# Performance work log

Hardware: AMD Instinct MI355X
Metric: run time of the kernel (lower is better)

The kernel has to match this reference:

```python
import jax, jax.numpy as jnp
import numpy as np

N, E = 10000, 100000   # nodes, edges
C = 64                 # sphere_channels
L2 = 9                 # (lmax+1)^2 with lmax=2
H, DH, DV = 8, 16, 16  # heads, alpha channels/head, value channels/head
EC = 64                # edge scalar channels
NRBF = 128             # radial basis size
ZMAX = 90              # max_num_elements


def setup_inputs() -> dict:
    key = jax.random.key(0)
    ks = jax.random.split(key, 12)
    inp = {}
    inp["node_embedding"] = jax.random.normal(ks[0], (N, L2, C), jnp.float32)
    inp["atomic_numbers"] = jax.random.randint(ks[1], (N,), 0, ZMAX)
    inp["edge_distance"] = jax.random.uniform(ks[2], (E,), jnp.float32)
    inp["edge_index"] = jax.random.randint(ks[3], (2, E), 0, N)
    # per-edge Wigner rotation into the edge-aligned SO(2) frame
    inp["wigner"] = jax.random.normal(ks[4], (E, L2, L2), jnp.float32) / np.sqrt(L2)
    # learned parameters
    inp["atom_emb"] = jax.random.normal(ks[5], (ZMAX, EC), jnp.float32) * 0.1
    inp["W_rbf"] = jax.random.normal(ks[6], (NRBF, EC), jnp.float32) / np.sqrt(NRBF)
    inp["W_gate"] = jax.random.normal(ks[7], (EC, H * DH), jnp.float32) / np.sqrt(EC)
    inp["W_msg"] = jax.random.normal(ks[8], (2 * C, H * DH), jnp.float32) / np.sqrt(2 * C)
    inp["alpha_vec"] = jax.random.normal(ks[9], (H, DH), jnp.float32) / np.sqrt(DH)
    inp["W_val"] = jax.random.normal(ks[10], (H * DH, H * DV), jnp.float32) / np.sqrt(H * DH)
    inp["W_out"] = jax.random.normal(ks[11], (H * DV, 1), jnp.float32) / np.sqrt(H * DV)
    return inp


def reference(node_embedding, atomic_numbers, edge_distance, edge_index, wigner,
              atom_emb, W_rbf, W_gate, W_msg, alpha_vec, W_val, W_out):
    src, dst = edge_index[0], edge_index[1]
    # --- edge scalar embedding: gaussian RBF of distance + endpoint atom embeddings ---
    centers = jnp.linspace(0.0, 1.0, NRBF, dtype=node_embedding.dtype)
    width = 1.0 / NRBF
    rbf = jnp.exp(-((edge_distance[:, None] - centers) ** 2) / (2.0 * width * width))  # [E, NRBF]
    edge_scalar = jax.nn.silu(rbf @ W_rbf + atom_emb[atomic_numbers[src]] + atom_emb[atomic_numbers[dst]])  # [E, EC]
    gate = jax.nn.silu(edge_scalar @ W_gate)  # [E, H*DH]
    # --- gather endpoint embeddings and rotate into edge frame (SO3 rotation) ---
    x_s = jnp.einsum('eij,ejc->eic', wigner, node_embedding[src])  # [E, L2, C]
    x_t = jnp.einsum('eij,ejc->eic', wigner, node_embedding[dst])  # [E, L2, C]
    msg = jnp.concatenate([x_s, x_t], axis=-1) @ W_msg            # [E, L2, H*DH]
    msg = msg * gate[:, None, :]
    # --- attention logits from the invariant (l=0) component ---
    a = msg[:, 0, :].reshape(E, H, DH)
    logits = jnp.einsum('ehd,hd->eh', jax.nn.leaky_relu(a, 0.2), alpha_vec)  # [E, H]
    # --- softmax over incoming edges of each destination node ---
    m = jax.ops.segment_max(logits, dst, num_segments=N)  # [N, H]
    ex = jnp.exp(logits - m[dst])
    den = jax.ops.segment_sum(ex, dst, num_segments=N)
    attn = ex / (den[dst] + 1e-9)  # [E, H]
    # --- attention-weighted values, rotate back, scatter-sum to nodes ---
    v = (msg @ W_val).reshape(E, L2, H, DV)
    v = v * attn[:, None, :, None]
    v = jnp.einsum('eji,ejhv->eihv', wigner, v).reshape(E, L2, H * DV)  # rotate back (R^T)
    node_out = jax.ops.segment_sum(v, dst, num_segments=N)  # [N, L2, H*DV]
    out = node_out @ W_out                                   # [N, L2, 1]
    forces = out[:, 1:4, 0]                                  # narrow(1,1,3).view(-1,3)
    return forces
```

## Files before the change

kernel.cpp:

```cpp
#include <hip/hip_runtime.h>
#include <hip/hip_bf16.h>

#define NN 10000
#define NE 100000

typedef __attribute__((ext_vector_type(8))) short short8v;
typedef __attribute__((ext_vector_type(4))) float float4v;

__device__ __forceinline__ unsigned int enc_f(float f) {
  unsigned int u = __float_as_uint(f);
  return (u & 0x80000000u) ? ~u : (u | 0x80000000u);
}
__device__ __forceinline__ float dec_f(unsigned int u) {
  return __uint_as_float((u & 0x80000000u) ? (u & 0x7fffffffu) : ~u);
}
__device__ __forceinline__ float silu_f(float x) {
  return x / (1.0f + __expf(-x));
}
__device__ __forceinline__ void f32_hilo(float x, short& h, short& l) {
  __hip_bfloat16 bh = __float2bfloat16(x);
  float r = x - __bfloat162float(bh);
  __hip_bfloat16 bl = __float2bfloat16(r);
  h = __builtin_bit_cast(short, bh);
  l = __builtin_bit_cast(short, bl);
}
#define MFMA16(a, b, c) __builtin_amdgcn_mfma_f32_16x16x32_bf16(a, b, c, 0, 0, 0)

__global__ void prep_kernel(const float* __restrict__ W_msg, const float* __restrict__ W_val,
                            const float* __restrict__ W_out, const float* __restrict__ W_rbf,
                            const float* __restrict__ W_gate,
                            float* __restrict__ Q,
                            short* __restrict__ Wp1h, short* __restrict__ Wp1l,
                            short* __restrict__ Wp2h, short* __restrict__ Wp2l,
                            short* __restrict__ Wp3h, short* __restrict__ Wp3l,
                            short* __restrict__ Wp4h, short* __restrict__ Wp4l) {
  int i = blockIdx.x * blockDim.x + threadIdx.x;
  if (i < 1024) {
    int c = i >> 3, h = i & 7;
    float s = 0.0f;
#pragma unroll
    for (int dv = 0; dv < 16; ++dv)
      s += W_val[c * 128 + h * 16 + dv] * W_out[h * 16 + dv];
    Q[c * 8 + h] = s;
  }
  const float* W; short* ph; short* pl; int KF, Nw, local; bool tr = false;
  if (i < 8192)       { W = W_rbf;  ph = Wp1h; pl = Wp1l; KF = 4; Nw = 64;  local = i; }
  else if (i < 16384) { W = W_gate; ph = Wp2h; pl = Wp2l; KF = 2; Nw = 128; local = i - 8192; }
  else if (i < 32768) { W = W_msg;  ph = Wp3h; pl = Wp3l; KF = 4; Nw = 128; local = i - 16384; }
  else                { W = W_msg;  ph = Wp4h; pl = Wp4l; KF = 4; Nw = 128; local = i - 32768; tr = true; }
  int tile = local >> 9;
  int ln = (local >> 3) & 63;
  int j = local & 7;
  int nt = tile / KF, kf = tile % KF;
  int k = kf * 32 + 8 * (ln >> 4) + j;
  int n = nt * 16 + (ln & 15);
  float w = tr ? W[n * 128 + k] : W[k * Nw + n];
  short h, lo;
  f32_hilo(w, h, lo);
  ph[local] = h;
  pl[local] = lo;
}

__global__ __launch_bounds__(256) void gather1_kernel(
    const float* __restrict__ nb, const int* __restrict__ ei,
    const float* __restrict__ wig, float* __restrict__ xc) {
  const int lane = threadIdx.x & 63;
  const int e = blockIdx.x * 4 + (threadIdx.x >> 6);
  int se = ei[e], de = ei[NE + e];
  const float* __restrict__ pw = wig + (size_t)e * 81;
  const float* __restrict__ ps = nb + (size_t)se * 576 + lane;
  const float* __restrict__ pt = nb + (size_t)de * 576 + lane;
  float vs[9], vt[9], wj[9];
#pragma unroll
  for (int j = 0; j < 9; ++j) {
    vs[j] = ps[j * 64];
    vt[j] = pt[j * 64];
    wj[j] = pw[j];
  }
  float xs = 0.0f, xt = 0.0f;
#pragma unroll
  for (int j = 0; j < 9; ++j) { xs += wj[j] * vs[j]; xt += wj[j] * vt[j]; }
  xc[(size_t)e * 128 + lane] = xs;
  xc[(size_t)e * 128 + 64 + lane] = xt;
}

__global__ __launch_bounds__(256, 3) void pass1_kernel(
    const int* __restrict__ zn, const float* __restrict__ dist,
    const int* __restrict__ ei, const float* __restrict__ aemb,
    const float* __restrict__ alpha, const float* __restrict__ xc,
    const short* __restrict__ Wp1h, const short* __restrict__ Wp1l,
    const short* __restrict__ Wp2h, const short* __restrict__ Wp2l,
    const short* __restrict__ Wp3h, const short* __restrict__ Wp3l,
    float* __restrict__ logits, unsigned int* __restrict__ m_enc,
    __hip_bfloat16* __restrict__ gate_ws) {
  __shared__ __attribute__((aligned(16))) float es_s[4][16][68];
  const int tid = threadIdx.x;
  const int lane = tid & 63;
  const int wid = tid >> 6;
  const int g = lane >> 4;
  const int col = lane & 15;
  const int e0 = (blockIdx.x * 4 + wid) * 16;

  int l16 = lane & 15;
  int ecl16 = (e0 + l16 < NE) ? e0 + l16 : NE - 1;
  int idx_v = 0;
  if (lane < 32) idx_v = ei[(lane < 16 ? 0 : NE) + ecl16];

  int ecol = e0 + col; if (ecol >= NE) ecol = NE - 1;
  const float d = dist[ecol];

  const float* __restrict__ xr = xc + (size_t)ecol * 128;
  float4v xv[4][2];
#pragma unroll
  for (int kf = 0; kf < 4; ++kf) {
    xv[kf][0] = *(const float4v*)(xr + kf * 32 + 8 * g);
    xv[kf][1] = *(const float4v*)(xr + kf * 32 + 8 * g + 4);
  }

  short8v a1h[4], a1l[4];
#pragma unroll
  for (int kf = 0; kf < 4; ++kf) {
#pragma unroll
    for (int j = 0; j < 8; ++j) {
      int k = kf * 32 + 8 * g + j;
      float t = d - (float)k * (1.0f / 127.0f);
      float v = __expf(-8192.0f * t * t);
      short h, lo; f32_hilo(v, h, lo);
      a1h[kf][j] = h; a1l[kf][j] = lo;
    }
  }

  const float4v z4 = {0.0f, 0.0f, 0.0f, 0.0f};

  float4v acc1[4];
#pragma unroll
  for (int nt = 0; nt < 4; ++nt) {
    float4v a = z4;
#pragma unroll
    for (int kf = 0; kf < 4; ++kf) {
      short8v bh = *(const short8v*)(Wp1h + ((nt * 4 + kf) * 64 + lane) * 8);
      short8v bl = *(const short8v*)(Wp1l + ((nt * 4 + kf) * 64 + lane) * 8);
      a = MFMA16(a1h[kf], bh, a);
      a = MFMA16(a1h[kf], bl, a);
      a = MFMA16(a1l[kf], bh, a);
    }
    acc1[nt] = a;
  }

  int dn_r[4];
#pragma unroll
  for (int r = 0; r < 4; ++r) {
    int sn = __shfl(idx_v, 4 * g + r);
    dn_r[r] = __shfl(idx_v, 16 + 4 * g + r);
    int zs = zn[sn], zd = zn[dn_r[r]];
#pragma unroll
    for (int nt = 0; nt < 4; ++nt) {
      float b = aemb[zs * 64 + nt * 16 + col] + aemb[zd * 64 + nt * 16 + col];
      es_s[wid][4 * g + r][nt * 16 + col] = silu_f(acc1[nt][r] + b);
    }
  }

  short8v a2h[2], a2l[2];
#pragma unroll
  for (int kf = 0; kf < 2; ++kf) {
    const float* p = &es_s[wid][col][kf * 32 + 8 * g];
    float4v v0 = *(const float4v*)p;
    float4v v1 = *(const float4v*)(p + 4);
#pragma unroll
    for (int j = 0; j < 4; ++j) {
      short h, lo;
      f32_hilo(v0[j], h, lo); a2h[kf][j] = h;     a2l[kf][j] = lo;
      f32_hilo(v1[j], h, lo); a2h[kf][4 + j] = h; a2l[kf][4 + j] = lo;
    }
  }

  float gate_r[8][4];
#pragma unroll
  for (int nt = 0; nt < 8; ++nt) {
    float4v a = z4;
#pragma unroll
    for (int kf = 0; kf < 2; ++kf) {
      short8v bh = *(const short8v*)(Wp2h + ((nt * 2 + kf) * 64 + lane) * 8);
      short8v bl = *(const short8v*)(Wp2l + ((nt * 2 + kf) * 64 + lane) * 8);
      a = MFMA16(a2h[kf], bh, a);
      a = MFMA16(a2h[kf], bl, a);
      a = MFMA16(a2l[kf], bh, a);
    }
#pragma unroll
    for (int r = 0; r < 4; ++r) {
      float gv = silu_f(a[r]);
      gate_r[nt][r] = gv;
      int er = e0 + 4 * g + r;
      if (er < NE)
        gate_ws[(size_t)er * 128 + nt * 16 + col] = __float2bfloat16(gv);
    }
  }

  short8v a3h[4], a3l[4];
#pragma unroll
  for (int kf = 0; kf < 4; ++kf) {
#pragma unroll
    for (int j = 0; j < 4; ++j) {
      short h, lo;
      f32_hilo(xv[kf][0][j], h, lo); a3h[kf][j] = h;     a3l[kf][j] = lo;
      f32_hilo(xv[kf][1][j], h, lo); a3h[kf][4 + j] = h; a3l[kf][4 + j] = lo;
    }
  }

#pragma unroll
  for (int nt = 0; nt < 8; ++nt) {
    float4v a = z4;
#pragma unroll
    for (int kf = 0; kf < 4; ++kf) {
      short8v bh = *(const short8v*)(Wp3h + ((nt * 4 + kf) * 64 + lane) * 8);
      short8v bl = *(const short8v*)(Wp3l + ((nt * 4 + kf) * 64 + lane) * 8);
      a = MFMA16(a3h[kf], bh, a);
      a = MFMA16(a3h[kf], bl, a);
      a = MFMA16(a3l[kf], bh, a);
    }
    float al = alpha[nt * 16 + col];
#pragma unroll
    for (int r = 0; r < 4; ++r) {
      float v = a[r] * gate_r[nt][r];
      v = v > 0.0f ? v : 0.2f * v;
      v *= al;
#pragma unroll
      for (int off = 1; off < 16; off <<= 1) v += __shfl_xor(v, off);
      int er = e0 + 4 * g + r;
      if (col == 0 && er < NE) {
        logits[(size_t)er * 8 + nt] = v;
        atomicMax(&m_enc[dn_r[r] * 8 + nt], enc_f(v));
      }
    }
  }
}

__global__ void pass2_kernel(const float* __restrict__ logits,
                             const int* __restrict__ ei,
                             const unsigned int* __restrict__ m_enc,
                             float* __restrict__ den) {
  int i = blockIdx.x * blockDim.x + threadIdx.x;
  if (i >= NE * 8) return;
  int e = i >> 3, h = i & 7;
  int dn = ei[NE + e];
  float mm = dec_f(m_enc[dn * 8 + h]);
  atomicAdd(&den[dn * 8 + h], __expf(logits[i] - mm));
}

__global__ __launch_bounds__(256, 3) void pass3a_kernel(
    const int* __restrict__ ei, const float* __restrict__ logits,
    const unsigned int* __restrict__ m_enc, const float* __restrict__ den,
    const __hip_bfloat16* __restrict__ gate_ws, const float* __restrict__ Q,
    const short* __restrict__ Wp4h, const short* __restrict__ Wp4l,
    float* __restrict__ t_ws) {
  __shared__ __attribute__((aligned(16))) float attn_s[4][16][8];
  __shared__ __attribute__((aligned(16))) float x_s[4][16][132];
  const int tid = threadIdx.x;
  const int lane = tid & 63;
  const int wid = tid >> 6;
  const int g = lane >> 4;
  const int col = lane & 15;
  const int e0 = (blockIdx.x * 4 + wid) * 16;

#pragma unroll
  for (int half = 0; half < 2; ++half) {
    int i = half * 64 + lane;
    int e = i >> 3, h = i & 7;
    int ec = e0 + e; if (ec >= NE) ec = NE - 1;
    int dn = ei[NE + ec];
    float l = logits[(size_t)ec * 8 + h];
    float mm = dec_f(m_enc[dn * 8 + h]);
    float dv = den[dn * 8 + h];
    attn_s[wid][e][h] = __expf(l - mm) / (dv + 1e-9f);
  }

  float q0[8], q1[8];
#pragma unroll
  for (int h = 0; h < 8; ++h) {
    q0[h] = Q[(2 * lane) * 8 + h];
    q1[h] = Q[(2 * lane + 1) * 8 + h];
  }
#pragma unroll 4
  for (int e = 0; e < 16; ++e) {
    int ec = e0 + e; if (ec >= NE) ec = NE - 1;
    float4v a0 = *(const float4v*)&attn_s[wid][e][0];
    float4v a1 = *(const float4v*)&attn_s[wid][e][4];
    float wv0 = 0.0f, wv1 = 0.0f;
#pragma unroll
    for (int h = 0; h < 4; ++h) {
      wv0 += q0[h] * a0[h] + q0[4 + h] * a1[h];
      wv1 += q1[h] * a0[h] + q1[4 + h] * a1[h];
    }
    unsigned int gp = *(const unsigned int*)(gate_ws + (size_t)ec * 128 + 2 * lane);
    float gg0 = __uint_as_float((gp & 0xffffu) << 16);
    float gg1 = __uint_as_float((gp & 0xffff0000u));
    float2 uu; uu.x = gg0 * wv0; uu.y = gg1 * wv1;
    *(float2*)&x_s[wid][e][2 * lane] = uu;
  }

  short8v ah[4], al[4];
#pragma unroll
  for (int kf = 0; kf < 4; ++kf) {
    const float* p = &x_s[wid][col][kf * 32 + 8 * g];
    float4v v0 = *(const float4v*)p;
    float4v v1 = *(const float4v*)(p + 4);
#pragma unroll
    for (int j = 0; j < 4; ++j) {
      short h, lo;
      f32_hilo(v0[j], h, lo); ah[kf][j] = h;     al[kf][j] = lo;
      f32_hilo(v1[j], h, lo); ah[kf][4 + j] = h; al[kf][4 + j] = lo;
    }
  }
  const float4v z4 = {0.0f, 0.0f, 0.0f, 0.0f};
#pragma unroll
  for (int nt = 0; nt < 8; ++nt) {
    float4v a = z4;
#pragma unroll
    for (int kf = 0; kf < 4; ++kf) {
      short8v bh = *(const short8v*)(Wp4h + ((nt * 4 + kf) * 64 + lane) * 8);
      short8v bl = *(const short8v*)(Wp4l + ((nt * 4 + kf) * 64 + lane) * 8);
      a = MFMA16(ah[kf], bh, a);
      a = MFMA16(ah[kf], bl, a);
      a = MFMA16(al[kf], bh, a);
    }
#pragma unroll
    for (int r = 0; r < 4; ++r) {
      int er = e0 + 4 * g + r;
      if (er < NE)
        t_ws[(size_t)er * 128 + nt * 16 + col] = a[r];
    }
  }
}

__global__ __launch_bounds__(256) void pass3b_kernel(
    const float* __restrict__ nb, const int* __restrict__ ei,
    const float* __restrict__ wig, const float* __restrict__ t_ws,
    float* __restrict__ out) {
  const int lane = threadIdx.x & 63;
  const int e = blockIdx.x * 4 + (threadIdx.x >> 6);
  int se = ei[e], de = ei[NE + e];
  float t0 = t_ws[(size_t)e * 128 + lane];
  float t1 = t_ws[(size_t)e * 128 + 64 + lane];
  const float* __restrict__ ps = nb + (size_t)se * 576 + lane;
  const float* __restrict__ pt = nb + (size_t)de * 576 + lane;
  float p[9];
#pragma unroll
  for (int j = 0; j < 9; ++j)
    p[j] = ps[j * 64] * t0 + pt[j * 64] * t1;
#pragma unroll
  for (int off = 1; off < 64; off <<= 1)
#pragma unroll
    for (int j = 0; j < 9; ++j) p[j] += __shfl_xor(p[j], off);

  const float* __restrict__ we = wig + (size_t)e * 81;
  int ls = lane < 9 ? lane : 8;
  float s_l = 0.0f;
#pragma unroll
  for (int jp = 0; jp < 9; ++jp) s_l += we[ls * 9 + jp] * p[jp];
  int lc = (lane >= 1 && lane <= 3) ? lane : 1;
  float f = 0.0f;
#pragma unroll
  for (int j = 0; j < 9; ++j)
    f += __shfl(s_l, j) * we[j * 9 + lc];
  if (lane >= 1 && lane <= 3)
    atomicAdd(&out[de * 3 + (lane - 1)], f);
}

extern "C" void kernel_launch(void* const* d_in, const int* in_sizes, int n_in,
                              void* d_out, int out_size, void* d_ws, size_t ws_size,
                              hipStream_t stream) {
  const float* nb = (const float*)d_in[0];
  const int* zn = (const int*)d_in[1];
  const float* dist = (const float*)d_in[2];
  const int* ei = (const int*)d_in[3];
  const float* wig = (const float*)d_in[4];
  const float* aemb = (const float*)d_in[5];
  const float* W_rbf = (const float*)d_in[6];
  const float* W_gate = (const float*)d_in[7];
  const float* W_msg = (const float*)d_in[8];
  const float* alpha = (const float*)d_in[9];
  const float* W_val = (const float*)d_in[10];
  const float* W_out = (const float*)d_in[11];
  float* out = (float*)d_out;

  char* p = (char*)d_ws;
  float* Q = (float*)p;                   p += 1024 * 4;
  unsigned int* m_enc = (unsigned int*)p; p += (size_t)NN * 8 * 4;
  float* den = (float*)p;                 p += (size_t)NN * 8 * 4;
  float* logits = (float*)p;              p += (size_t)NE * 8 * 4;
  __hip_bfloat16* gate_ws = (__hip_bfloat16*)p; p += (size_t)NE * 128 * 2;
  short* Wp1h = (short*)p; p += 8192 * 2;
  short* Wp1l = (short*)p; p += 8192 * 2;
  short* Wp2h = (short*)p; p += 8192 * 2;
  short* Wp2l = (short*)p; p += 8192 * 2;
  short* Wp3h = (short*)p; p += 16384 * 2;
  short* Wp3l = (short*)p; p += 16384 * 2;
  short* Wp4h = (short*)p; p += 16384 * 2;
  short* Wp4l = (short*)p; p += 16384 * 2;
  float* xc_ws = (float*)p;               p += (size_t)NE * 128 * 4;
  float* t_ws = xc_ws;

  hipMemsetAsync(d_out, 0, (size_t)NN * 3 * 4, stream);
  hipMemsetAsync(m_enc, 0, (size_t)NN * 8 * 4, stream);
  hipMemsetAsync(den, 0, (size_t)NN * 8 * 4, stream);

  prep_kernel<<<192, 256, 0, stream>>>(W_msg, W_val, W_out, W_rbf, W_gate, Q,
                                       Wp1h, Wp1l, Wp2h, Wp2l, Wp3h, Wp3l, Wp4h, Wp4l);
  gather1_kernel<<<NE / 4, 256, 0, stream>>>(nb, ei, wig, xc_ws);
  pass1_kernel<<<(NE + 63) / 64, 256, 0, stream>>>(zn, dist, ei, aemb, alpha, xc_ws,
                                                   Wp1h, Wp1l, Wp2h, Wp2l, Wp3h, Wp3l,
                                                   logits, m_enc, gate_ws);
  pass2_kernel<<<(NE * 8 + 255) / 256, 256, 0, stream>>>(logits, ei, m_enc, den);
  pass3a_kernel<<<(NE + 63) / 64, 256, 0, stream>>>(ei, logits, m_enc, den,
                                                    gate_ws, Q, Wp4h, Wp4l, t_ws);
  pass3b_kernel<<<NE / 4, 256, 0, stream>>>(nb, ei, wig, t_ws, out);
}
```

Before: 344.6 us.

## Precompute rotated Gram terms in gather and fuse pass3b into pass3

The gather kernel now computes the full rotated embedding for each edge. It writes the l=0 row as pre-split bf16 hi/lo pairs, and it writes the contraction of the rotated rows with Wigner columns 1..3 as a bf16 G tensor. This lets the final pass compute forces from G and the t-vector held in shared memory. The separate pass3b kernel, which re-gathered node embeddings and Wigner rows, is removed along with the t_ws round trip. This trades more FLOPs and an extra 768 B/edge of G writes in gather for removing a full endpoint re-gather, and it adds bf16 rounding on G.

```diff
diff --git a/kernel.cpp b/kernel.cpp
--- a/kernel.cpp
+++ b/kernel.cpp
@@ -5,6 +5,7 @@
 #define NE 100000
 
 typedef __attribute__((ext_vector_type(8))) short short8v;
+typedef __attribute__((ext_vector_type(4))) short short4v;
 typedef __attribute__((ext_vector_type(4))) float float4v;
 
 __device__ __forceinline__ unsigned int enc_f(float f) {
@@ -16,6 +17,9 @@
 }
 __device__ __forceinline__ float silu_f(float x) {
   return x / (1.0f + __expf(-x));
+}
+__device__ __forceinline__ float b2f(short s) {
+  return __uint_as_float(((unsigned int)(unsigned short)s) << 16);
 }
 __device__ __forceinline__ void f32_hilo(float x, short& h, short& l) {
   __hip_bfloat16 bh = __float2bfloat16(x);
@@ -23,6 +27,9 @@
   __hip_bfloat16 bl = __float2bfloat16(r);
   h = __builtin_bit_cast(short, bh);
   l = __builtin_bit_cast(short, bl);
+}
+__device__ __forceinline__ short f2bf(float x) {
+  return __builtin_bit_cast(short, __float2bfloat16(x));
 }
 #define MFMA16(a, b, c) __builtin_amdgcn_mfma_f32_16x16x32_bf16(a, b, c, 0, 0, 0)
 
@@ -63,31 +70,55 @@
 
 __global__ __launch_bounds__(256) void gather1_kernel(
     const float* __restrict__ nb, const int* __restrict__ ei,
-    const float* __restrict__ wig, float* __restrict__ xc) {
+    const float* __restrict__ wig, short* __restrict__ xch,
+    short* __restrict__ xcl, short* __restrict__ Gb) {
   const int lane = threadIdx.x & 63;
   const int e = blockIdx.x * 4 + (threadIdx.x >> 6);
   int se = ei[e], de = ei[NE + e];
   const float* __restrict__ pw = wig + (size_t)e * 81;
   const float* __restrict__ ps = nb + (size_t)se * 576 + lane;
   const float* __restrict__ pt = nb + (size_t)de * 576 + lane;
-  float vs[9], vt[9], wj[9];
+  float vs[9], vt[9];
 #pragma unroll
   for (int j = 0; j < 9; ++j) {
     vs[j] = ps[j * 64];
     vt[j] = pt[j * 64];
-    wj[j] = pw[j];
-  }
-  float xs = 0.0f, xt = 0.0f;
-#pragma unroll
-  for (int j = 0; j < 9; ++j) { xs += wj[j] * vs[j]; xt += wj[j] * vt[j]; }
-  xc[(size_t)e * 128 + lane] = xs;
-  xc[(size_t)e * 128 + 64 + lane] = xt;
+  }
+  float Gs0 = 0, Gs1 = 0, Gs2 = 0, Gt0 = 0, Gt1 = 0, Gt2 = 0;
+#pragma unroll
+  for (int j = 0; j < 9; ++j) {
+    float row[9];
+#pragma unroll
+    for (int jp = 0; jp < 9; ++jp) row[jp] = pw[j * 9 + jp];
+    float xs = 0.0f, xt = 0.0f;
+#pragma unroll
+    for (int jp = 0; jp < 9; ++jp) { xs += row[jp] * vs[jp]; xt += row[jp] * vt[jp]; }
+    if (j == 0) {
+      short h, l;
+      f32_hilo(xs, h, l);
+      xch[(size_t)e * 128 + lane] = h;
+      xcl[(size_t)e * 128 + lane] = l;
+      f32_hilo(xt, h, l);
+      xch[(size_t)e * 128 + 64 + lane] = h;
+      xcl[(size_t)e * 128 + 64 + lane] = l;
+    }
+    Gs0 += row[1] * xs; Gs1 += row[2] * xs; Gs2 += row[3] * xs;
+    Gt0 += row[1] * xt; Gt1 += row[2] * xt; Gt2 += row[3] * xt;
+  }
+  short* gp = Gb + (size_t)e * 384 + lane;
+  gp[0]       = f2bf(Gs0);
+  gp[64]      = f2bf(Gs1);
+  gp[128]     = f2bf(Gs2);
+  gp[192]     = f2bf(Gt0);
+  gp[256]     = f2bf(Gt1);
+  gp[320]     = f2bf(Gt2);
 }
 
 __global__ __launch_bounds__(256, 3) void pass1_kernel(
     const int* __restrict__ zn, const float* __restrict__ dist,
     const int* __restrict__ ei, const float* __restrict__ aemb,
-    const float* __restrict__ alpha, const float* __restrict__ xc,
+    const float* __restrict__ alpha,
+    const short* __restrict__ xch, const short* __restrict__ xcl,
     const short* __restrict__ Wp1h, const short* __restrict__ Wp1l,
     const short* __restrict__ Wp2h, const short* __restrict__ Wp2l,
     const short* __restrict__ Wp3h, const short* __restrict__ Wp3l,
@@ -109,12 +140,13 @@
   int ecol = e0 + col; if (ecol >= NE) ecol = NE - 1;
   const float d = dist[ecol];
 
-  const float* __restrict__ xr = xc + (size_t)ecol * 128;
-  float4v xv[4][2];
+  const short* ph = xch + (size_t)ecol * 128 + 8 * g;
+  const short* pl = xcl + (size_t)ecol * 128 + 8 * g;
+  short8v a3h[4], a3l[4];
 #pragma unroll
   for (int kf = 0; kf < 4; ++kf) {
-    xv[kf][0] = *(const float4v*)(xr + kf * 32 + 8 * g);
-    xv[kf][1] = *(const float4v*)(xr + kf * 32 + 8 * g + 4);
+    a3h[kf] = *(const short8v*)(ph + kf * 32);
+    a3l[kf] = *(const short8v*)(pl + kf * 32);
   }
 
   short8v a1h[4], a1l[4];
@@ -193,17 +225,6 @@
       int er = e0 + 4 * g + r;
       if (er < NE)
         gate_ws[(size_t)er * 128 + nt * 16 + col] = __float2bfloat16(gv);
-    }
-  }
-
-  short8v a3h[4], a3l[4];
-#pragma unroll
-  for (int kf = 0; kf < 4; ++kf) {
-#pragma unroll
-    for (int j = 0; j < 4; ++j) {
-      short h, lo;
-      f32_hilo(xv[kf][0][j], h, lo); a3h[kf][j] = h;     a3l[kf][j] = lo;
-      f32_hilo(xv[kf][1][j], h, lo); a3h[kf][4 + j] = h; a3l[kf][4 + j] = lo;
     }
   }
 
@@ -247,12 +268,12 @@
   atomicAdd(&den[dn * 8 + h], __expf(logits[i] - mm));
 }
 
-__global__ __launch_bounds__(256, 3) void pass3a_kernel(
+__global__ __launch_bounds__(256, 3) void pass3_kernel(
     const int* __restrict__ ei, const float* __restrict__ logits,
     const unsigned int* __restrict__ m_enc, const float* __restrict__ den,
     const __hip_bfloat16* __restrict__ gate_ws, const float* __restrict__ Q,
     const short* __restrict__ Wp4h, const short* __restrict__ Wp4l,
-    float* __restrict__ t_ws) {
+    const short* __restrict__ Gb, float* __restrict__ out) {
   __shared__ __attribute__((aligned(16))) float attn_s[4][16][8];
   __shared__ __attribute__((aligned(16))) float x_s[4][16][132];
   const int tid = threadIdx.x;
@@ -324,46 +345,37 @@
       a = MFMA16(al[kf], bh, a);
     }
 #pragma unroll
-    for (int r = 0; r < 4; ++r) {
-      int er = e0 + 4 * g + r;
-      if (er < NE)
-        t_ws[(size_t)er * 128 + nt * 16 + col] = a[r];
-    }
-  }
-}
-
-__global__ __launch_bounds__(256) void pass3b_kernel(
-    const float* __restrict__ nb, const int* __restrict__ ei,
-    const float* __restrict__ wig, const float* __restrict__ t_ws,
-    float* __restrict__ out) {
-  const int lane = threadIdx.x & 63;
-  const int e = blockIdx.x * 4 + (threadIdx.x >> 6);
-  int se = ei[e], de = ei[NE + e];
-  float t0 = t_ws[(size_t)e * 128 + lane];
-  float t1 = t_ws[(size_t)e * 128 + 64 + lane];
-  const float* __restrict__ ps = nb + (size_t)se * 576 + lane;
-  const float* __restrict__ pt = nb + (size_t)de * 576 + lane;
-  float p[9];
-#pragma unroll
-  for (int j = 0; j < 9; ++j)
-    p[j] = ps[j * 64] * t0 + pt[j * 64] * t1;
-#pragma unroll
-  for (int off = 1; off < 64; off <<= 1)
-#pragma unroll
-    for (int j = 0; j < 9; ++j) p[j] += __shfl_xor(p[j], off);
-
-  const float* __restrict__ we = wig + (size_t)e * 81;
-  int ls = lane < 9 ? lane : 8;
-  float s_l = 0.0f;
-#pragma unroll
-  for (int jp = 0; jp < 9; ++jp) s_l += we[ls * 9 + jp] * p[jp];
-  int lc = (lane >= 1 && lane <= 3) ? lane : 1;
-  float f = 0.0f;
-#pragma unroll
-  for (int j = 0; j < 9; ++j)
-    f += __shfl(s_l, j) * we[j * 9 + lc];
-  if (lane >= 1 && lane <= 3)
-    atomicAdd(&out[de * 3 + (lane - 1)], f);
+    for (int r = 0; r < 4; ++r)
+      x_s[wid][4 * g + r][nt * 16 + col] = a[r];
+  }
+
+  const int cg = col * 4;
+#pragma unroll
+  for (int it = 0; it < 4; ++it) {
+    int e = it * 4 + g;
+    int eu = e0 + e;
+    bool valid = eu < NE;
+    int ec = valid ? eu : NE - 1;
+    int de = ei[NE + ec];
+    float4v t0 = *(const float4v*)&x_s[wid][e][cg];
+    float4v t1 = *(const float4v*)&x_s[wid][e][64 + cg];
+    const short* gp = Gb + (size_t)ec * 384 + cg;
+    float p[3];
+#pragma unroll
+    for (int i = 0; i < 3; ++i) {
+      short4v gs = *(const short4v*)(gp + i * 64);
+      short4v gt = *(const short4v*)(gp + (3 + i) * 64);
+      p[i] = b2f(gs[0]) * t0[0] + b2f(gs[1]) * t0[1] + b2f(gs[2]) * t0[2] + b2f(gs[3]) * t0[3] +
+             b2f(gt[0]) * t1[0] + b2f(gt[1]) * t1[1] + b2f(gt[2]) * t1[2] + b2f(gt[3]) * t1[3];
+    }
+#pragma unroll
+    for (int i = 0; i < 3; ++i)
+#pragma unroll
+      for (int off = 1; off < 16; off <<= 1) p[i] += __shfl_xor(p[i], off);
+    float pv = (col == 1) ? p[0] : ((col == 2) ? p[1] : p[2]);
+    if (valid && col >= 1 && col <= 3)
+      atomicAdd(&out[de * 3 + (col - 1)], pv);
+  }
 }
 
 extern "C" void kernel_launch(void* const* d_in, const int* in_sizes, int n_in,
@@ -397,8 +409,9 @@
   short* Wp3l = (short*)p; p += 16384 * 2;
   short* Wp4h = (short*)p; p += 16384 * 2;
   short* Wp4l = (short*)p; p += 16384 * 2;
-  float* xc_ws = (float*)p;               p += (size_t)NE * 128 * 4;
-  float* t_ws = xc_ws;
+  short* xch = (short*)p;                 p += (size_t)NE * 128 * 2;
+  short* xcl = (short*)p;                 p += (size_t)NE * 128 * 2;
+  short* Gb = (short*)p;                  p += (size_t)NE * 384 * 2;
 
   hipMemsetAsync(d_out, 0, (size_t)NN * 3 * 4, stream);
   hipMemsetAsync(m_enc, 0, (size_t)NN * 8 * 4, stream);
@@ -406,12 +419,12 @@
 
   prep_kernel<<<192, 256, 0, stream>>>(W_msg, W_val, W_out, W_rbf, W_gate, Q,
                                        Wp1h, Wp1l, Wp2h, Wp2l, Wp3h, Wp3l, Wp4h, Wp4l);
-  gather1_kernel<<<NE / 4, 256, 0, stream>>>(nb, ei, wig, xc_ws);
-  pass1_kernel<<<(NE + 63) / 64, 256, 0, stream>>>(zn, dist, ei, aemb, alpha, xc_ws,
+  gather1_kernel<<<NE / 4, 256, 0, stream>>>(nb, ei, wig, xch, xcl, Gb);
+  pass1_kernel<<<(NE + 63) / 64, 256, 0, stream>>>(zn, dist, ei, aemb, alpha,
+                                                   xch, xcl,
                                                    Wp1h, Wp1l, Wp2h, Wp2l, Wp3h, Wp3l,
                                                    logits, m_enc, gate_ws);
   pass2_kernel<<<(NE * 8 + 255) / 256, 256, 0, stream>>>(logits, ei, m_enc, den);
-  pass3a_kernel<<<(NE + 63) / 64, 256, 0, stream>>>(ei, logits, m_enc, den,
-                                                    gate_ws, Q, Wp4h, Wp4l, t_ws);
-  pass3b_kernel<<<NE / 4, 256, 0, stream>>>(nb, ei, wig, t_ws, out);
-}
+  pass3_kernel<<<(NE + 63) / 64, 256, 0, stream>>>(ei, logits, m_enc, den,
+                                                   gate_ws, Q, Wp4h, Wp4l, Gb, out);
+}
```

New measurement: 315.3 us. -8.5%, faster.
